# Kernel optimization log

Measured on AMD Instinct MI355X. Metric: run time of the kernel, lower is better.

The kernel has to match this reference:

```python
import jax, jax.numpy as jnp
import numpy as np

B, N, D, U = 256, 256, 256, 256


def setup_inputs() -> dict:
    key = jax.random.key(0)
    k1, k2, k3, k4 = jax.random.split(key, 4)
    inputs = jax.random.normal(k1, (B, N, D), jnp.float32)
    # chain tree per batch: parent of node i is i+1; node N-1 is the root (-1)
    parents_row = np.concatenate([np.arange(1, N), [-1]]).astype(np.int32)
    parents = jnp.tile(jnp.asarray(parents_row)[None, :], (B, 1))
    # post order 0..N-1 is a valid bottom-up topological order for the chain
    post_orders = jnp.tile(jnp.arange(N, dtype=jnp.int32)[None, :], (B, 1))
    glorot = lambda k, sh: jax.random.normal(k, sh, jnp.float32) * np.sqrt(2.0 / (sh[0] + sh[1]))
    return dict(
        inputs=inputs,
        parents=parents,
        post_orders=post_orders,
        x_fiou_kernel=glorot(k2, (D, 4 * U)),
        h_f_kernel=glorot(k3, (U, U)),
        h_iou_kernel=glorot(k4, (U, 3 * U)),
        fiou_bias=jnp.zeros((4 * U,), jnp.float32),
    )


def reference(inputs, parents, post_orders, x_fiou_kernel, h_f_kernel, h_iou_kernel, fiou_bias):
    Bq, Nn, _ = inputs.shape
    units = h_f_kernel.shape[0]
    b_idx = jnp.arange(Bq)

    # precompute input projections: [B,N,4U] -> f part [B,N,U], iou part [B,N,3U]
    fiou_xb = jnp.einsum('bnd,dk->bnk', inputs, x_fiou_kernel) + fiou_bias
    f_xb, iou_xb = fiou_xb[..., :units], fiou_xb[..., units:]

    order_mask = post_orders >= 0
    po = jnp.maximum(post_orders, 0)
    sorted_parents = jnp.take_along_axis(parents, po, axis=1)  # [B,O]

    def step(carry, xs):
        hs, csh, gcs = carry
        tgt, par_raw, om = xs  # [B] each
        pm = (par_raw >= 0) & om
        par = jnp.maximum(par_raw, 0)
        # aggregate node: child-sum h through iou kernel
        iou = iou_xb[b_idx, tgt] + csh[b_idx, tgt] @ h_iou_kernel  # [B,3U]
        i, o, u = jnp.split(iou, 3, axis=1)
        mem = jax.nn.sigmoid(i) * jnp.tanh(u) + gcs[b_idx, tgt]
        out = jax.nn.sigmoid(o) * jnp.tanh(mem)
        # gate memory by parent's forget gate
        gated = jax.nn.sigmoid(out @ h_f_kernel + f_xb[b_idx, par]) * mem
        omf = om[:, None].astype(out.dtype)
        pmf = pm[:, None].astype(out.dtype)
        hs = hs.at[b_idx, tgt].add(out * omf)
        csh = csh.at[b_idx, par].add(out * pmf)
        gcs = gcs.at[b_idx, par].add(gated * pmf)
        return (hs, csh, gcs), None

    init = tuple(jnp.zeros((Bq, Nn, units), inputs.dtype) for _ in range(3))
    xs = (po.T, sorted_parents.T, order_mask.T)  # scan over post-order steps
    (hs, _, _), _ = jax.lax.scan(step, init, xs)
    return hs
```

## Files before the change

### kernel.cpp

```cpp
#include <hip/hip_runtime.h>
#include <hip/hip_bf16.h>

#define Bq 256
#define Nn 256
#define Dd 256
#define Uu 256

using bf16 = __hip_bfloat16;

typedef __attribute__((ext_vector_type(8))) short s16x8;
typedef __attribute__((ext_vector_type(4))) float f32x4;

__device__ __forceinline__ float bu2f(unsigned short u) {
  return __uint_as_float(((unsigned)u) << 16);
}
__device__ __forceinline__ unsigned short f2bu(float f) {
  union { bf16 h; unsigned short u; } c; c.h = __float2bfloat16(f); return c.u;
}
__device__ __forceinline__ float sigf(float x) { return 1.0f / (1.0f + __expf(-x)); }
__device__ __forceinline__ float tanh_(float x) { return 2.0f / (1.0f + __expf(-2.0f * x)) - 1.0f; }
__device__ __forceinline__ s16x8 asv(uint4 x) {
  union { uint4 u; s16x8 v; } c; c.u = x; return c.v;
}
#define MFMA16(a, b, c) __builtin_amdgcn_mfma_f32_16x16x32_bf16(a, b, c, 0, 0, 0)

__global__ __launch_bounds__(256) void prep_weights(
    const float* __restrict__ hiou, const float* __restrict__ hf,
    bf16* __restrict__ wiouB, bf16* __restrict__ wfB) {
  int idx = blockIdx.x * 256 + threadIdx.x;
  int e = idx & 7, l = (idx >> 3) & 63, kt = (idx >> 9) & 7;
  int k = kt * 32 + (l >> 4) * 8 + e;
  if (idx < 196608) {
    int nt = (idx >> 12) & 15, g = idx >> 16;
    wiouB[idx] = __float2bfloat16(hiou[k * 768 + g * 256 + nt * 16 + (l & 15)]);
  } else {
    int t = idx - 196608;
    int nt = (t >> 12) & 15;
    wfB[t] = __float2bfloat16(hf[k * 256 + nt * 16 + (l & 15)]);
  }
}

__global__ __launch_bounds__(256) void prep_xw(
    const float* __restrict__ xw, bf16* __restrict__ xwHi, bf16* __restrict__ xwLo) {
  int idx = blockIdx.x * 256 + threadIdx.x;
  int e = idx & 7, l = (idx >> 3) & 63, kt = (idx >> 9) & 7, nt = idx >> 12;
  int k = kt * 32 + (l >> 4) * 8 + e;
  float v = xw[k * 1024 + nt * 16 + (l & 15)];
  bf16 h = __float2bfloat16(v);
  xwHi[idx] = h;
  xwLo[idx] = __float2bfloat16(v - (float)h);
}

__global__ __launch_bounds__(256) void prep_nd(
    const int* __restrict__ parents, const int* __restrict__ post,
    unsigned* __restrict__ ndg) {
  int idx = blockIdx.x * 256 + threadIdx.x;
  int b = idx >> 8, t = idx & 255;
  int po = post[b * 256 + t];
  int om = po >= 0;
  int tgt = om ? po : 0;
  int praw = parents[b * 256 + tgt];
  int pm = (praw >= 0) && om;
  int par = praw >= 0 ? praw : 0;
  unsigned word = (unsigned)(tgt & 255) | ((unsigned)(par & 255) << 8) |
                  ((unsigned)om << 16) | ((unsigned)pm << 17);
  ndg[(b >> 4) * 4096 + t * 16 + (b & 15)] = word;
}

extern __shared__ char smem[];

__global__ __launch_bounds__(256) void xproj(
    const float* __restrict__ x, const float* __restrict__ w,
    const float* __restrict__ bias, bf16* __restrict__ out) {
  __shared__ float xs[Dd][16];
  const int tid = threadIdx.x;
  const int row0 = blockIdx.x * 16;
  for (int i = 0; i < 16; ++i) {
    int idx = i * 256 + tid;
    int r = idx >> 8, k = idx & 255;
    xs[k][r] = x[(size_t)(row0 + r) * Dd + k];
  }
  __syncthreads();
  const int c0 = tid * 4;
  float4 bv = *(const float4*)(bias + c0);
  float acc[16][4];
#pragma unroll
  for (int r = 0; r < 16; ++r) {
    acc[r][0] = bv.x; acc[r][1] = bv.y; acc[r][2] = bv.z; acc[r][3] = bv.w;
  }
  for (int k = 0; k < Dd; ++k) {
    float4 wv = *(const float4*)(w + (size_t)k * 1024 + c0);
    const float4* xr = (const float4*)xs[k];
    float4 x0 = xr[0], x1 = xr[1], x2 = xr[2], x3 = xr[3];
    float xv[16] = {x0.x, x0.y, x0.z, x0.w, x1.x, x1.y, x1.z, x1.w,
                    x2.x, x2.y, x2.z, x2.w, x3.x, x3.y, x3.z, x3.w};
#pragma unroll
    for (int r = 0; r < 16; ++r) {
      acc[r][0] += xv[r] * wv.x;
      acc[r][1] += xv[r] * wv.y;
      acc[r][2] += xv[r] * wv.z;
      acc[r][3] += xv[r] * wv.w;
    }
  }
#pragma unroll
  for (int r = 0; r < 16; ++r) {
    union { ushort4 u4; bf16 b[4]; } pk;
    pk.b[0] = __float2bfloat16(acc[r][0]);
    pk.b[1] = __float2bfloat16(acc[r][1]);
    pk.b[2] = __float2bfloat16(acc[r][2]);
    pk.b[3] = __float2bfloat16(acc[r][3]);
    *(ushort4*)(&out[(size_t)(row0 + r) * 1024 + c0]) = pk.u4;
  }
}

#define XP_LDS (2 * 64 * 264 * 2)
__global__ __launch_bounds__(512, 2) void xproj2(
    const float* __restrict__ x, const unsigned short* __restrict__ xwHi,
    const unsigned short* __restrict__ xwLo, const float* __restrict__ bias,
    unsigned short* __restrict__ out) {
  unsigned short* a_hi = (unsigned short*)smem;
  unsigned short* a_lo = a_hi + 64 * 264;
  const int tid = threadIdx.x;
  const int w = tid >> 6, l = tid & 63;
  const int lm = l & 15, lq = l >> 4;
  const size_t row0 = (size_t)blockIdx.x * 64;

  {
    int r = tid >> 3, c0 = (tid & 7) * 32;
    const float* src = x + (row0 + r) * 256 + c0;
#pragma unroll
    for (int c = 0; c < 32; c += 4) {
      float4 v = *(const float4*)(src + c);
      unsigned short h0 = f2bu(v.x), h1 = f2bu(v.y), h2 = f2bu(v.z), h3 = f2bu(v.w);
      ushort4 hv = {h0, h1, h2, h3};
      ushort4 lv = {f2bu(v.x - bu2f(h0)), f2bu(v.y - bu2f(h1)),
                    f2bu(v.z - bu2f(h2)), f2bu(v.w - bu2f(h3))};
      *(ushort4*)&a_hi[r * 264 + c0 + c] = hv;
      *(ushort4*)&a_lo[r * 264 + c0 + c] = lv;
    }
  }
  __syncthreads();

  const uint4* bh = (const uint4*)xwHi;
  const uint4* bl = (const uint4*)xwLo;
  f32x4 acc[8][4];
#pragma unroll
  for (int nt = 0; nt < 8; ++nt) {
    float b = bias[(w * 8 + nt) * 16 + lm];
#pragma unroll
    for (int rt = 0; rt < 4; ++rt) acc[nt][rt] = {b, b, b, b};
  }
  for (int kt = 0; kt < 8; ++kt) {
    uint4 Bh[8], Bl[8];
#pragma unroll
    for (int nt = 0; nt < 8; ++nt) {
      int f = ((w * 8 + nt) * 8 + kt) * 64 + l;
      Bh[nt] = bh[f];
      Bl[nt] = bl[f];
    }
    s16x8 Ah[4], Al[4];
#pragma unroll
    for (int rt = 0; rt < 4; ++rt) {
      Ah[rt] = asv(*(const uint4*)&a_hi[(rt * 16 + lm) * 264 + kt * 32 + lq * 8]);
      Al[rt] = asv(*(const uint4*)&a_lo[(rt * 16 + lm) * 264 + kt * 32 + lq * 8]);
    }
#pragma unroll
    for (int nt = 0; nt < 8; ++nt)
#pragma unroll
      for (int rt = 0; rt < 4; ++rt) {
        acc[nt][rt] = MFMA16(Ah[rt], asv(Bh[nt]), acc[nt][rt]);
        acc[nt][rt] = MFMA16(Ah[rt], asv(Bl[nt]), acc[nt][rt]);
        acc[nt][rt] = MFMA16(Al[rt], asv(Bh[nt]), acc[nt][rt]);
      }
  }
#pragma unroll
  for (int nt = 0; nt < 8; ++nt)
#pragma unroll
    for (int rt = 0; rt < 4; ++rt)
#pragma unroll
      for (int r = 0; r < 4; ++r) {
        size_t row = row0 + rt * 16 + lq * 4 + r;
        out[row * 1024 + (w * 8 + nt) * 16 + lm] = f2bu(acc[nt][rt][r]);
      }
}

#define LDH 264
#define SCAN_LDS (131072 + 2 * 16 * LDH * 2)

__global__ __launch_bounds__(512, 2) void scan3(
    const unsigned short* __restrict__ fiou, const unsigned short* __restrict__ wiouB,
    const unsigned short* __restrict__ wfB, const unsigned* __restrict__ ndg,
    float* __restrict__ X, float* __restrict__ gcs) {
  unsigned short* i_lds = (unsigned short*)smem;
  unsigned short* h_lds = (unsigned short*)(smem + 131072);
  unsigned short* o_lds = h_lds + 16 * LDH;
  __shared__ int okf;

  const int tid = threadIdx.x;
  const int w = tid >> 6, l = tid & 63;
  const int lm = l & 15, lq = l >> 4;
  const int b = blockIdx.x;
  const int jj = 32 * w + lm;
  const int nt0 = 2 * w;
  const bool act = (lq == 0);
  const bool arow = (lm == 0);

  if (tid == 0) okf = 1;
  const uint4* wp  = (const uint4*)wiouB;
  const uint4* wf4 = (const uint4*)wfB;
  {
    uint4* d = (uint4*)i_lds;
    for (int i = tid; i < 8192; i += 512) d[i] = wp[i];
  }
  for (int i = tid; i < 2 * 16 * LDH; i += 512) h_lds[i] = 0;
  uint4 wor[2][8], wur[2][8], wfr[2][8];
#pragma unroll
  for (int ts = 0; ts < 2; ++ts)
#pragma unroll
    for (int kt = 0; kt < 8; ++kt) {
      wor[ts][kt] = wp[((16 + (nt0 + ts)) * 8 + kt) * 64 + l];
      wur[ts][kt] = wp[((32 + (nt0 + ts)) * 8 + kt) * 64 + l];
      wfr[ts][kt] = wf4[((nt0 + ts) * 8 + kt) * 64 + l];
    }
  const unsigned* ndb = ndg + (b >> 4) * 4096 + (b & 15);
  __syncthreads();

  if (tid < 256) {
    unsigned exp_ = (tid < 255)
        ? ((unsigned)tid | ((unsigned)(tid + 1) << 8) | 0x30000u)
        : (255u | 0x10000u);
    if (ndb[tid * 16] != exp_) atomicAnd(&okf, 0);
  }
  __syncthreads();

  const uint4* il4 = (const uint4*)i_lds;
  const f32x4 z4 = {0.f, 0.f, 0.f, 0.f};
  const size_t fb = ((size_t)b) << 18;
  const size_t xb = ((size_t)b) << 16;

  if (okf != 0) {
    unsigned short* obA = h_lds;
    unsigned short* obW = o_lds;
    float gc_[2] = {0.f, 0.f};
    unsigned short rxi[2], rxo[2], rxu[2], rxf[2];
    if (act) {
#pragma unroll
      for (int ts = 0; ts < 2; ++ts) {
        int j = jj + ts * 16;
        rxi[ts] = fiou[fb + 256 + j];
        rxo[ts] = fiou[fb + 512 + j];
        rxu[ts] = fiou[fb + 768 + j];
        rxf[ts] = fiou[fb + 1024 + j];
      }
    }

    for (int t = 0; t < Nn; ++t) {
      f32x4 aI[2] = {z4, z4}, aO[2] = {z4, z4}, aU[2] = {z4, z4};
#pragma unroll
      for (int kt = 0; kt < 8; ++kt) {
        uint4 av = {0u, 0u, 0u, 0u};
        if (arow) av = *(const uint4*)&obA[kt * 32 + lq * 8];
        s16x8 a = asv(av);
#pragma unroll
        for (int ts = 0; ts < 2; ++ts) {
          aI[ts] = MFMA16(a, asv(il4[((nt0 + ts) * 8 + kt) * 64 + l]), aI[ts]);
          aO[ts] = MFMA16(a, asv(wor[ts][kt]), aO[ts]);
          aU[ts] = MFMA16(a, asv(wur[ts][kt]), aU[ts]);
        }
      }

      float mem_[2], out_[2];
      if (act) {
#pragma unroll
        for (int ts = 0; ts < 2; ++ts) {
          float I  = aI[ts][0] + bu2f(rxi[ts]);
          float O  = aO[ts][0] + bu2f(rxo[ts]);
          float Uv = aU[ts][0] + bu2f(rxu[ts]);
          float memv = sigf(I) * tanh_(Uv) + gc_[ts];
          float outv = sigf(O) * tanh_(memv);
          mem_[ts] = memv;
          out_[ts] = outv;
          obW[jj + ts * 16] = f2bu(outv);
        }
      }
      __syncthreads();

      const int tgtN = (t < Nn - 1) ? t + 1 : t;
      if (act) {
#pragma unroll
        for (int ts = 0; ts < 2; ++ts)
          X[xb + (size_t)t * 256 + jj + ts * 16] = out_[ts];
        size_t fr = fb + (size_t)tgtN * 1024;
#pragma unroll
        for (int ts = 0; ts < 2; ++ts) {
          int j = jj + ts * 16;
          rxi[ts] = fiou[fr + 256 + j];
          rxo[ts] = fiou[fr + 512 + j];
          rxu[ts] = fiou[fr + 768 + j];
        }
      }

      f32x4 aF[2] = {z4, z4};
#pragma unroll
      for (int kt = 0; kt < 8; ++kt) {
        uint4 av = {0u, 0u, 0u, 0u};
        if (arow) av = *(const uint4*)&obW[kt * 32 + lq * 8];
        s16x8 a = asv(av);
#pragma unroll
        for (int ts = 0; ts < 2; ++ts)
          aF[ts] = MFMA16(a, asv(wfr[ts][kt]), aF[ts]);
      }

      if (act) {
#pragma unroll
        for (int ts = 0; ts < 2; ++ts) {
          float AF = aF[ts][0] + bu2f(rxf[ts]);
          gc_[ts] = sigf(AF) * mem_[ts];
        }
        int parN = (tgtN < 255) ? tgtN + 1 : 0;
        size_t fp = fb + (size_t)parN * 1024;
#pragma unroll
        for (int ts = 0; ts < 2; ++ts)
          rxf[ts] = fiou[fp + jj + ts * 16];
      }

      unsigned short* tmp = obA; obA = obW; obW = tmp;
    }
  } else {
    for (int t = 0; t < Nn; ++t) {
      unsigned nd_ = ndb[t * 16];
      int tgt = nd_ & 255, par = (nd_ >> 8) & 255;

      if (tid < 256)
        h_lds[tid] = f2bu(X[xb + (size_t)tgt * 256 + tid]);

      unsigned short rxi[2], rxo[2], rxu[2], rxf[2];
      float rgc[2], xold[2], gold[2];
      if (act) {
        size_t ft = fb + (size_t)tgt * 1024;
        size_t fp = fb + (size_t)par * 1024;
#pragma unroll
        for (int ts = 0; ts < 2; ++ts) {
          int j = jj + ts * 16;
          rxi[ts] = fiou[ft + 256 + j];
          rxo[ts] = fiou[ft + 512 + j];
          rxu[ts] = fiou[ft + 768 + j];
          rxf[ts] = fiou[fp + j];
          rgc[ts]  = gcs[xb + (size_t)tgt * 256 + j];
          xold[ts] = X[xb + (size_t)par * 256 + j];
          gold[ts] = gcs[xb + (size_t)par * 256 + j];
        }
      }
      __syncthreads();

      f32x4 aI[2] = {z4, z4}, aO[2] = {z4, z4}, aU[2] = {z4, z4};
#pragma unroll
      for (int kt = 0; kt < 8; ++kt) {
        uint4 av = *(const uint4*)&h_lds[lm * LDH + kt * 32 + lq * 8];
        s16x8 a = asv(av);
#pragma unroll
        for (int ts = 0; ts < 2; ++ts) {
          aI[ts] = MFMA16(a, asv(il4[((nt0 + ts) * 8 + kt) * 64 + l]), aI[ts]);
          aO[ts] = MFMA16(a, asv(wor[ts][kt]), aO[ts]);
          aU[ts] = MFMA16(a, asv(wur[ts][kt]), aU[ts]);
        }
      }

      float mem_[2], out_[2];
      if (act) {
#pragma unroll
        for (int ts = 0; ts < 2; ++ts) {
          float I  = aI[ts][0] + bu2f(rxi[ts]);
          float O  = aO[ts][0] + bu2f(rxo[ts]);
          float Uv = aU[ts][0] + bu2f(rxu[ts]);
          float memv = sigf(I) * tanh_(Uv) + rgc[ts];
          float outv = sigf(O) * tanh_(memv);
          mem_[ts] = memv;
          out_[ts] = outv;
          o_lds[jj + ts * 16] = f2bu(outv);
        }
      }
      __syncthreads();

      f32x4 aF[2] = {z4, z4};
#pragma unroll
      for (int kt = 0; kt < 8; ++kt) {
        uint4 av = *(const uint4*)&o_lds[lm * LDH + kt * 32 + lq * 8];
        s16x8 a = asv(av);
#pragma unroll
        for (int ts = 0; ts < 2; ++ts)
          aF[ts] = MFMA16(a, asv(wfr[ts][kt]), aF[ts]);
      }

      if (act) {
#pragma unroll
        for (int ts = 0; ts < 2; ++ts) {
          int j = jj + ts * 16;
          float AF = aF[ts][0] + bu2f(rxf[ts]);
          float gated = sigf(AF) * mem_[ts];
          if (nd_ & 0x10000u) X[xb + (size_t)tgt * 256 + j] = out_[ts];
          if (nd_ & 0x20000u) {
            X[xb + (size_t)par * 256 + j] = xold[ts] + out_[ts];
            gcs[xb + (size_t)par * 256 + j] = gold[ts] + gated;
          }
        }
      }
      __syncthreads();
    }
  }
}

extern "C" void kernel_launch(void* const* d_in, const int* in_sizes, int n_in,
                              void* d_out, int out_size, void* d_ws, size_t ws_size,
                              hipStream_t stream) {
  const float* inputs = (const float*)d_in[0];
  const int* parents  = (const int*)d_in[1];
  const int* post     = (const int*)d_in[2];
  const float* xw     = (const float*)d_in[3];
  const float* hf     = (const float*)d_in[4];
  const float* hiou   = (const float*)d_in[5];
  const float* bias   = (const float*)d_in[6];
  float* X = (float*)d_out;

  char* ws = (char*)d_ws;
  bf16* fiou     = (bf16*)ws;
  float* gcs     = (float*)(ws + (size_t)134217728);
  bf16* wiouB    = (bf16*)(ws + (size_t)201326592);
  bf16* wfB      = (bf16*)(ws + (size_t)201719808);
  unsigned* ndg  = (unsigned*)(ws + (size_t)201850880);
  bf16* xwHi     = (bf16*)(ws + (size_t)202113024);
  bf16* xwLo     = (bf16*)(ws + (size_t)202637312);
  const bool big_ws = ws_size >= (size_t)202113024 + 2 * 524288;

  hipMemsetAsync(X, 0, (size_t)Bq * Nn * Uu * sizeof(float), stream);
  hipMemsetAsync(gcs, 0, (size_t)Bq * Nn * Uu * sizeof(float), stream);

  hipFuncSetAttribute(reinterpret_cast<const void*>(scan3),
                      hipFuncAttributeMaxDynamicSharedMemorySize, SCAN_LDS);

  prep_weights<<<1024, 256, 0, stream>>>(hiou, hf, wiouB, wfB);
  prep_nd<<<256, 256, 0, stream>>>(parents, post, ndg);
  if (big_ws) {
    hipFuncSetAttribute(reinterpret_cast<const void*>(xproj2),
                        hipFuncAttributeMaxDynamicSharedMemorySize, XP_LDS);
    prep_xw<<<1024, 256, 0, stream>>>(xw, xwHi, xwLo);
    xproj2<<<(Bq * Nn) / 64, 512, XP_LDS, stream>>>(
        inputs, (const unsigned short*)xwHi, (const unsigned short*)xwLo,
        bias, (unsigned short*)fiou);
  } else {
    xproj<<<(Bq * Nn) / 16, 256, 0, stream>>>(inputs, xw, bias, (bf16*)fiou);
  }
  scan3<<<256, 512, SCAN_LDS, stream>>>((const unsigned short*)fiou,
                                        (const unsigned short*)wiouB,
                                        (const unsigned short*)wfB,
                                        ndg, X, gcs);
}
```

Baseline: 1.644 ms.

## Fuse per-step iou and forget matmuls into one pass over the chain output

```diff
diff --git a/kernel.cpp b/kernel.cpp
--- a/kernel.cpp
+++ b/kernel.cpp
@@ -239,9 +239,10 @@
   const size_t xb = ((size_t)b) << 16;
 
   if (okf != 0) {
-    unsigned short* obA = h_lds;
-    unsigned short* obW = o_lds;
+    unsigned short* bufA = h_lds;
+    unsigned short* bufB = o_lds;
     float gc_[2] = {0.f, 0.f};
+    f32x4 accI[2] = {z4, z4}, accO[2] = {z4, z4}, accU[2] = {z4, z4};
     unsigned short rxi[2], rxo[2], rxu[2], rxf[2];
     if (act) {
 #pragma unroll
@@ -255,32 +256,18 @@
     }
 
     for (int t = 0; t < Nn; ++t) {
-      f32x4 aI[2] = {z4, z4}, aO[2] = {z4, z4}, aU[2] = {z4, z4};
-#pragma unroll
-      for (int kt = 0; kt < 8; ++kt) {
-        uint4 av = {0u, 0u, 0u, 0u};
-        if (arow) av = *(const uint4*)&obA[kt * 32 + lq * 8];
-        s16x8 a = asv(av);
-#pragma unroll
-        for (int ts = 0; ts < 2; ++ts) {
-          aI[ts] = MFMA16(a, asv(il4[((nt0 + ts) * 8 + kt) * 64 + l]), aI[ts]);
-          aO[ts] = MFMA16(a, asv(wor[ts][kt]), aO[ts]);
-          aU[ts] = MFMA16(a, asv(wur[ts][kt]), aU[ts]);
-        }
-      }
-
       float mem_[2], out_[2];
       if (act) {
 #pragma unroll
         for (int ts = 0; ts < 2; ++ts) {
-          float I  = aI[ts][0] + bu2f(rxi[ts]);
-          float O  = aO[ts][0] + bu2f(rxo[ts]);
-          float Uv = aU[ts][0] + bu2f(rxu[ts]);
+          float I  = accI[ts][0] + bu2f(rxi[ts]);
+          float O  = accO[ts][0] + bu2f(rxo[ts]);
+          float Uv = accU[ts][0] + bu2f(rxu[ts]);
           float memv = sigf(I) * tanh_(Uv) + gc_[ts];
           float outv = sigf(O) * tanh_(memv);
           mem_[ts] = memv;
           out_[ts] = outv;
-          obW[jj + ts * 16] = f2bu(outv);
+          bufA[jj + ts * 16] = f2bu(outv);
         }
       }
       __syncthreads();
@@ -302,13 +289,19 @@
 
       f32x4 aF[2] = {z4, z4};
 #pragma unroll
+      for (int ts = 0; ts < 2; ++ts) { accI[ts] = z4; accO[ts] = z4; accU[ts] = z4; }
+#pragma unroll
       for (int kt = 0; kt < 8; ++kt) {
         uint4 av = {0u, 0u, 0u, 0u};
-        if (arow) av = *(const uint4*)&obW[kt * 32 + lq * 8];
+        if (arow) av = *(const uint4*)&bufA[kt * 32 + lq * 8];
         s16x8 a = asv(av);
 #pragma unroll
-        for (int ts = 0; ts < 2; ++ts)
-          aF[ts] = MFMA16(a, asv(wfr[ts][kt]), aF[ts]);
+        for (int ts = 0; ts < 2; ++ts) {
+          aF[ts]   = MFMA16(a, asv(wfr[ts][kt]), aF[ts]);
+          accI[ts] = MFMA16(a, asv(il4[((nt0 + ts) * 8 + kt) * 64 + l]), accI[ts]);
+          accO[ts] = MFMA16(a, asv(wor[ts][kt]), accO[ts]);
+          accU[ts] = MFMA16(a, asv(wur[ts][kt]), accU[ts]);
+        }
       }
 
       if (act) {
@@ -324,7 +317,7 @@
           rxf[ts] = fiou[fp + jj + ts * 16];
       }
 
-      unsigned short* tmp = obA; obA = obW; obW = tmp;
+      unsigned short* tmp = bufA; bufA = bufB; bufB = tmp;
     }
   } else {
     for (int t = 0; t < Nn; ++t) {
```

Result: faster. 1.562 ms (-5.0%).
